# Kernel tuning notes

Measured on AMD Instinct MI355X. Metric: run time of the kernel, lower is better.

Reference implementation:

```python
import jax, jax.numpy as jnp
import numpy as np

N_NODES = 100000
N_EDGES = 1600000
IN_DIM = 256
HID = 128
ALPHA = 0.1
K_STEPS = 10


def setup_inputs() -> dict:
    key = jax.random.key(0)
    ks = jax.random.split(key, 10)
    x = jax.random.normal(ks[0], (N_NODES, IN_DIM), dtype=jnp.float32)
    edge_index = jax.random.randint(ks[1], (2, N_EDGES), 0, N_NODES, dtype=jnp.int64)
    s = 0.02
    W1 = jax.random.normal(ks[2], (HID, IN_DIM), dtype=jnp.float32) * s
    b1 = jnp.zeros((HID,), dtype=jnp.float32)
    W2 = jax.random.normal(ks[3], (HID, HID), dtype=jnp.float32) * s
    b2 = jnp.zeros((HID,), dtype=jnp.float32)
    W3 = jax.random.normal(ks[4], (HID, HID), dtype=jnp.float32) * s
    b3 = jnp.zeros((HID,), dtype=jnp.float32)
    Wo = jax.random.normal(ks[5], (1, HID), dtype=jnp.float32) * s
    bo = jnp.zeros((1,), dtype=jnp.float32)
    return {"x": x, "edge_index": edge_index, "W1": W1, "b1": b1,
            "W2": W2, "b2": b2, "W3": W3, "b3": b3, "Wo": Wo, "bo": bo}


def _gcn_norm(edge_index, num_nodes):
    # add self-loops, then symmetric normalization 1/sqrt(deg_i * deg_j)
    loop = jnp.arange(num_nodes, dtype=edge_index.dtype)
    src = jnp.concatenate([edge_index[0], loop])
    dst = jnp.concatenate([edge_index[1], loop])
    ones = jnp.ones(src.shape[0], dtype=jnp.float32)
    deg = jax.ops.segment_sum(ones, dst, num_segments=num_nodes)
    dinv = jnp.where(deg > 0, jax.lax.rsqrt(deg), 0.0)
    norm = dinv[src] * dinv[dst]
    return src, dst, norm


def reference(x, edge_index, W1, b1, W2, b2, W3, b3, Wo, bo):
    # MLP encoder (dropout=0 -> identity in eval)
    h = jax.nn.relu(x @ W1.T + b1)
    h = jax.nn.relu(h @ W2.T + b2)
    h = jax.nn.relu(h @ W3.T + b3)
    # APPNP propagation: h <- (1-alpha) * A_hat h + alpha * h0
    n = x.shape[0]
    src, dst, norm = _gcn_norm(edge_index, n)
    h0 = h
    for _ in range(K_STEPS):
        msg = norm[:, None] * h[src]            # [E+N, HID]
        agg = jax.ops.segment_sum(msg, dst, num_segments=n)
        h = (1.0 - ALPHA) * agg + ALPHA * h0
    out = h @ Wo.T + bo                          # [N, 1]
    return out.squeeze(-1)
```

## Files before the change

kernel.cpp:

```cpp
#include <hip/hip_runtime.h>

#define NN   100000
#define NE   1600000
#define IND  256
#define HIDD 128
#define BCAP 64
#define NPART 196
#define SCAP 10240
#define APITCH 40
#define HPITCH 136

typedef __attribute__((ext_vector_type(8))) short short8v;
typedef __attribute__((ext_vector_type(4))) float f32x4;

__device__ inline unsigned packbf2(float x, float y) {
  unsigned xb = __float_as_uint(x);
  unsigned yb = __float_as_uint(y);
  xb += 0x7fffu + ((xb >> 16) & 1u);
  yb += 0x7fffu + ((yb >> 16) & 1u);
  return (xb >> 16) | (yb & 0xffff0000u);
}
__device__ inline unsigned short bf16r(float x) {
  unsigned b = __float_as_uint(x);
  b += 0x7fffu + ((b >> 16) & 1u);
  return (unsigned short)(b >> 16);
}

__global__ void wcvt_all(const float* __restrict__ W1, const float* __restrict__ W2,
                         const float* __restrict__ W3, unsigned* __restrict__ W1b,
                         unsigned* __restrict__ W2b, unsigned* __restrict__ W3b) {
  int i = blockIdx.x * 256 + threadIdx.x;
  const float* src; unsigned* dst; int off;
  if (i < 16384)      { src = W1; dst = W1b; off = i; }
  else if (i < 24576) { src = W2; dst = W2b; off = i - 16384; }
  else                { src = W3; dst = W3b; off = i - 24576; }
  float2 v = ((const float2*)src)[off];
  dst[off] = packbf2(v.x, v.y);
}

__global__ __launch_bounds__(256, 8) void fill_phaseA(
    const int* __restrict__ src, const int* __restrict__ dst,
    int* __restrict__ gcur, unsigned* __restrict__ sbuf)
{
  __shared__ int hist[NPART];
  __shared__ int lofs[NPART];
  const int tid = threadIdx.x;
  const int base = blockIdx.x * 2048;
  for (int i = tid; i < NPART; i += 256) hist[i] = 0;
  __syncthreads();
  int d[8], s[8];
#pragma unroll
  for (int i = 0; i < 8; ++i) {
    int e = base + i * 256 + tid;
    bool v = e < NE;
    d[i] = v ? dst[e] : -1;
    s[i] = v ? src[e] : 0;
    if (v) atomicAdd(&hist[d[i] >> 9], 1);
  }
  __syncthreads();
  for (int i = tid; i < NPART; i += 256)
    lofs[i] = hist[i] ? atomicAdd(&gcur[i], hist[i]) : 0;
  __syncthreads();
#pragma unroll
  for (int i = 0; i < 8; ++i) {
    if (d[i] >= 0) {
      int p = d[i] >> 9;
      int q = atomicAdd(&lofs[p], 1);
      if (q < SCAP)
        sbuf[(size_t)p * SCAP + q] = ((unsigned)(d[i] & 511) << 17) | (unsigned)s[i];
    }
  }
}

__global__ __launch_bounds__(256, 8) void fill_phaseB(
    const unsigned* __restrict__ sbuf, const int* __restrict__ gcur,
    int* __restrict__ colbuk, int* __restrict__ deg, float* __restrict__ dinv)
{
  __shared__ int lcur[512];
  const int tid = threadIdx.x;
  const int b = blockIdx.x;
  for (int i = tid; i < 512; i += 256) lcur[i] = 0;
  __syncthreads();
  int cnt = min(gcur[b], SCAP);
  const unsigned* sp = sbuf + (size_t)b * SCAP;
  for (int i = tid; i < cnt; i += 256) {
    unsigned u = sp[i];
    int dloc = (int)(u >> 17);
    int s = (int)(u & 0x1FFFFu);
    int pos = atomicAdd(&lcur[dloc], 1);
    if (pos < BCAP) colbuk[(size_t)((b << 9) + dloc) * BCAP + pos] = s;
  }
  __syncthreads();
  for (int i = tid; i < 512; i += 256) {
    int node = (b << 9) + i;
    if (node < NN) {
      int dg = lcur[i];
      deg[node] = dg;
      dinv[node] = rsqrtf((float)(dg + 1));
    }
  }
}

__global__ __launch_bounds__(256) void enc_fused(
    const float* __restrict__ x,
    const unsigned short* __restrict__ W1b, const float* __restrict__ b1,
    const unsigned short* __restrict__ W2b, const float* __restrict__ b2,
    const unsigned short* __restrict__ W3b, const float* __restrict__ b3,
    const float* __restrict__ Wo, const float* __restrict__ dinv,
    float* __restrict__ z, float* __restrict__ va)
{
  __shared__ unsigned short hbuf[64 * HPITCH];
  __shared__ float zsh[2][64];
  unsigned short* lA = hbuf;
  const int tid = threadIdx.x;
  const int lane = tid & 63, wid = tid >> 6;
  const int wr = wid >> 1, wc = wid & 1;
  const int bm = blockIdx.x * 64;
  const int lr = lane & 15, lg = lane >> 4;

  f32x4 acc[2][4];
#pragma unroll
  for (int i = 0; i < 2; ++i)
#pragma unroll
    for (int j = 0; j < 4; ++j) acc[i][j] = (f32x4){0.f, 0.f, 0.f, 0.f};

  for (int k0 = 0; k0 < IND; k0 += 32) {
    {
      int rr = tid >> 2, g = tid & 3;
      int grow = bm + rr;
      float4 v0 = make_float4(0.f, 0.f, 0.f, 0.f), v1 = v0;
      if (grow < NN) {
        const float* ap = x + (size_t)grow * IND + k0 + g * 8;
        v0 = ((const float4*)ap)[0]; v1 = ((const float4*)ap)[1];
      }
      uint4 pk;
      pk.x = packbf2(v0.x, v0.y); pk.y = packbf2(v0.z, v0.w);
      pk.z = packbf2(v1.x, v1.y); pk.w = packbf2(v1.z, v1.w);
      *(uint4*)&lA[rr * APITCH + g * 8] = pk;
    }
    __syncthreads();
    {
      short8v a[2], b[4];
#pragma unroll
      for (int i = 0; i < 2; ++i)
        a[i] = *(const short8v*)&lA[(wr * 32 + i * 16 + lr) * APITCH + lg * 8];
#pragma unroll
      for (int j = 0; j < 4; ++j)
        b[j] = *(const short8v*)&W1b[(size_t)(wc * 64 + j * 16 + lr) * IND + k0 + lg * 8];
#pragma unroll
      for (int i = 0; i < 2; ++i)
#pragma unroll
        for (int j = 0; j < 4; ++j)
          acc[i][j] = __builtin_amdgcn_mfma_f32_16x16x32_bf16(a[i], b[j], acc[i][j], 0, 0, 0);
    }
    __syncthreads();
  }
#pragma unroll
  for (int i = 0; i < 2; ++i)
#pragma unroll
    for (int e = 0; e < 4; ++e) {
      int lrow = wr * 32 + i * 16 + lg * 4 + e;
#pragma unroll
      for (int j = 0; j < 4; ++j) {
        int cc = wc * 64 + j * 16 + lr;
        hbuf[lrow * HPITCH + cc] = bf16r(fmaxf(acc[i][j][e] + b1[cc], 0.f));
      }
    }
  __syncthreads();

#pragma unroll
  for (int i = 0; i < 2; ++i)
#pragma unroll
    for (int j = 0; j < 4; ++j) acc[i][j] = (f32x4){0.f, 0.f, 0.f, 0.f};
  for (int k0 = 0; k0 < HIDD; k0 += 32) {
    short8v a[2], b[4];
#pragma unroll
    for (int i = 0; i < 2; ++i)
      a[i] = *(const short8v*)&hbuf[(wr * 32 + i * 16 + lr) * HPITCH + k0 + lg * 8];
#pragma unroll
    for (int j = 0; j < 4; ++j)
      b[j] = *(const short8v*)&W2b[(size_t)(wc * 64 + j * 16 + lr) * HIDD + k0 + lg * 8];
#pragma unroll
    for (int i = 0; i < 2; ++i)
#pragma unroll
      for (int j = 0; j < 4; ++j)
        acc[i][j] = __builtin_amdgcn_mfma_f32_16x16x32_bf16(a[i], b[j], acc[i][j], 0, 0, 0);
  }
  __syncthreads();
#pragma unroll
  for (int i = 0; i < 2; ++i)
#pragma unroll
    for (int e = 0; e < 4; ++e) {
      int lrow = wr * 32 + i * 16 + lg * 4 + e;
#pragma unroll
      for (int j = 0; j < 4; ++j) {
        int cc = wc * 64 + j * 16 + lr;
        hbuf[lrow * HPITCH + cc] = bf16r(fmaxf(acc[i][j][e] + b2[cc], 0.f));
      }
    }
  __syncthreads();

#pragma unroll
  for (int i = 0; i < 2; ++i)
#pragma unroll
    for (int j = 0; j < 4; ++j) acc[i][j] = (f32x4){0.f, 0.f, 0.f, 0.f};
  for (int k0 = 0; k0 < HIDD; k0 += 32) {
    short8v a[2], b[4];
#pragma unroll
    for (int i = 0; i < 2; ++i)
      a[i] = *(const short8v*)&hbuf[(wr * 32 + i * 16 + lr) * HPITCH + k0 + lg * 8];
#pragma unroll
    for (int j = 0; j < 4; ++j)
      b[j] = *(const short8v*)&W3b[(size_t)(wc * 64 + j * 16 + lr) * HIDD + k0 + lg * 8];
#pragma unroll
    for (int i = 0; i < 2; ++i)
#pragma unroll
      for (int j = 0; j < 4; ++j)
        acc[i][j] = __builtin_amdgcn_mfma_f32_16x16x32_bf16(a[i], b[j], acc[i][j], 0, 0, 0);
  }
  float wv[4];
#pragma unroll
  for (int j = 0; j < 4; ++j) wv[j] = Wo[wc * 64 + j * 16 + lr];
  if (tid < 128) { zsh[tid >> 6][tid & 63] = 0.f; }
  __syncthreads();
#pragma unroll
  for (int i = 0; i < 2; ++i)
#pragma unroll
    for (int e = 0; e < 4; ++e) {
      float part = 0.f;
#pragma unroll
      for (int j = 0; j < 4; ++j) {
        int cc = wc * 64 + j * 16 + lr;
        part += fmaxf(acc[i][j][e] + b3[cc], 0.f) * wv[j];
      }
#pragma unroll
      for (int off = 8; off > 0; off >>= 1) part += __shfl_down(part, off, 16);
      if (lr == 0) zsh[wc][wr * 32 + i * 16 + lg * 4 + e] = part;
    }
  __syncthreads();
  if (tid < 64) {
    int row = bm + tid;
    if (row < NN) {
      float zv = zsh[0][tid] + zsh[1][tid];
      z[row] = zv;
      va[row] = dinv[row] * zv;
    }
  }
}

template<int LAST>
__global__ __launch_bounds__(256, 8) void appnp_sstep(
    const float* __restrict__ vin, const float* __restrict__ z,
    const float* __restrict__ dinv, const int* __restrict__ deg,
    const int* __restrict__ colbuk, float* __restrict__ vout,
    const float* __restrict__ bo, float* __restrict__ out)
{
  int tid = threadIdx.x;
  int sl = tid & 15;
  int node = blockIdx.x * 16 + (tid >> 4);
  if (node >= NN) return;
  int m = min(deg[node], BCAP);
  float val = (sl == 0) ? vin[node] : 0.f;
  for (int j = sl; j < m; j += 16)
    val += vin[colbuk[(size_t)node * BCAP + j]];
#pragma unroll
  for (int off = 8; off > 0; off >>= 1) val += __shfl_down(val, off, 16);
  if (sl == 0) {
    float di = dinv[node];
    float s = 0.9f * di * val + 0.1f * z[node];
    if (LAST) out[node] = s + bo[0];
    else vout[node] = di * s;
  }
}

extern "C" void kernel_launch(void* const* d_in, const int* in_sizes, int n_in,
                              void* d_out, int out_size, void* d_ws, size_t ws_size,
                              hipStream_t stream) {
  const float* x   = (const float*)d_in[0];
  const int*   ei  = (const int*)d_in[1];
  const float* W1  = (const float*)d_in[2];
  const float* b1  = (const float*)d_in[3];
  const float* W2  = (const float*)d_in[4];
  const float* b2  = (const float*)d_in[5];
  const float* W3  = (const float*)d_in[6];
  const float* b3  = (const float*)d_in[7];
  const float* Wo  = (const float*)d_in[8];
  const float* bo  = (const float*)d_in[9];
  float* out = (float*)d_out;

  const int* srcv = ei;
  const int* dstv = ei + NE;

  int*      colbuk = (int*)d_ws;
  unsigned* sbuf   = (unsigned*)(colbuk + (size_t)NN * BCAP);
  int*      gcur   = (int*)(sbuf + (size_t)NPART * SCAP);
  int*      deg    = gcur + NPART;
  float*    dinv   = (float*)(deg + NN);
  float*    zbuf   = dinv + NN;
  float*    va     = zbuf + NN;
  float*    vb     = va + NN;
  unsigned* W1b    = (unsigned*)(vb + NN);
  unsigned* W2b    = W1b + 16384;
  unsigned* W3b    = W2b + 8192;

  hipMemsetAsync(gcur, 0, NPART * 4, stream);

  wcvt_all<<<128, 256, 0, stream>>>(W1, W2, W3, W1b, W2b, W3b);

  fill_phaseA<<<(NE + 2047) / 2048, 256, 0, stream>>>(srcv, dstv, gcur, sbuf);
  fill_phaseB<<<NPART, 256, 0, stream>>>(sbuf, gcur, colbuk, deg, dinv);

  const int ng = (NN + 63) / 64;
  enc_fused<<<ng, 256, 0, stream>>>(x, (unsigned short*)W1b, b1,
                                    (unsigned short*)W2b, b2,
                                    (unsigned short*)W3b, b3, Wo, dinv,
                                    zbuf, va);

  int ssb = (NN + 15) / 16;
  float* cur = va; float* nxt = vb;
  for (int k = 0; k < 9; ++k) {
    appnp_sstep<0><<<ssb, 256, 0, stream>>>(cur, zbuf, dinv, deg, colbuk,
                                            nxt, nullptr, nullptr);
    float* t = cur; cur = nxt; nxt = t;
  }
  appnp_sstep<1><<<ssb, 256, 0, stream>>>(cur, zbuf, dinv, deg, colbuk,
                                          nullptr, bo, out);
}
```

Measured before the change: 223.8 us.

## Fuse encoder MLP with edge-bucketing phase A into one interleaved launch

Merges the encoder MLP kernel and the first edge-partitioning kernel into one launch. Every third block does edge histogram/scatter work and the other two run MLP tiles, so memory-bound scatter overlaps with MFMA-bound encoder work. The encoder no longer depends on dinv. The dinv*z scaling moves into fill_phaseB, which now runs after the encoder. The fused kernel carries both kernels' shared memory and register needs, which may lower occupancy for the scatter blocks.

```diff
diff --git a/kernel.cpp b/kernel.cpp
--- a/kernel.cpp
+++ b/kernel.cpp
@@ -9,6 +9,8 @@
 #define SCAP 10240
 #define APITCH 40
 #define HPITCH 136
+#define NGE  1563
+#define NFA  782
 
 typedef __attribute__((ext_vector_type(8))) short short8v;
 typedef __attribute__((ext_vector_type(4))) float f32x4;
@@ -38,43 +40,191 @@
   dst[off] = packbf2(v.x, v.y);
 }
 
-__global__ __launch_bounds__(256, 8) void fill_phaseA(
+__global__ __launch_bounds__(256) void enc_fillA(
+    const float* __restrict__ x,
+    const unsigned short* __restrict__ W1b, const float* __restrict__ b1,
+    const unsigned short* __restrict__ W2b, const float* __restrict__ b2,
+    const unsigned short* __restrict__ W3b, const float* __restrict__ b3,
+    const float* __restrict__ Wo, float* __restrict__ z,
     const int* __restrict__ src, const int* __restrict__ dst,
     int* __restrict__ gcur, unsigned* __restrict__ sbuf)
 {
+  __shared__ unsigned short hbuf[64 * HPITCH];
+  __shared__ float zsh[2][64];
   __shared__ int hist[NPART];
   __shared__ int lofs[NPART];
   const int tid = threadIdx.x;
-  const int base = blockIdx.x * 2048;
-  for (int i = tid; i < NPART; i += 256) hist[i] = 0;
-  __syncthreads();
-  int d[8], s[8];
-#pragma unroll
-  for (int i = 0; i < 8; ++i) {
-    int e = base + i * 256 + tid;
-    bool v = e < NE;
-    d[i] = v ? dst[e] : -1;
-    s[i] = v ? src[e] : 0;
-    if (v) atomicAdd(&hist[d[i] >> 9], 1);
-  }
-  __syncthreads();
-  for (int i = tid; i < NPART; i += 256)
-    lofs[i] = hist[i] ? atomicAdd(&gcur[i], hist[i]) : 0;
-  __syncthreads();
-#pragma unroll
-  for (int i = 0; i < 8; ++i) {
-    if (d[i] >= 0) {
-      int p = d[i] >> 9;
-      int q = atomicAdd(&lofs[p], 1);
-      if (q < SCAP)
-        sbuf[(size_t)p * SCAP + q] = ((unsigned)(d[i] & 511) << 17) | (unsigned)s[i];
-    }
+  const int bid = blockIdx.x;
+  const int r3v = bid % 3;
+
+  if (r3v == 2) {
+    int fi = bid / 3;
+    const int base = fi * 2048;
+    for (int i = tid; i < NPART; i += 256) hist[i] = 0;
+    __syncthreads();
+    int d[8], s[8];
+#pragma unroll
+    for (int i = 0; i < 8; ++i) {
+      int e = base + i * 256 + tid;
+      bool v = e < NE;
+      d[i] = v ? dst[e] : -1;
+      s[i] = v ? src[e] : 0;
+      if (v) atomicAdd(&hist[d[i] >> 9], 1);
+    }
+    __syncthreads();
+    for (int i = tid; i < NPART; i += 256)
+      lofs[i] = hist[i] ? atomicAdd(&gcur[i], hist[i]) : 0;
+    __syncthreads();
+#pragma unroll
+    for (int i = 0; i < 8; ++i) {
+      if (d[i] >= 0) {
+        int p = d[i] >> 9;
+        int q = atomicAdd(&lofs[p], 1);
+        if (q < SCAP)
+          sbuf[(size_t)p * SCAP + q] = ((unsigned)(d[i] & 511) << 17) | (unsigned)s[i];
+      }
+    }
+    return;
+  }
+
+  const int gb = (bid / 3) * 2 + r3v;
+  if (gb >= NGE) return;
+  unsigned short* lA = hbuf;
+  const int lane = tid & 63, wid = tid >> 6;
+  const int wr = wid >> 1, wc = wid & 1;
+  const int bm = gb * 64;
+  const int lr = lane & 15, lg = lane >> 4;
+
+  f32x4 acc[2][4];
+#pragma unroll
+  for (int i = 0; i < 2; ++i)
+#pragma unroll
+    for (int j = 0; j < 4; ++j) acc[i][j] = (f32x4){0.f, 0.f, 0.f, 0.f};
+
+  for (int k0 = 0; k0 < IND; k0 += 32) {
+    {
+      int rr = tid >> 2, g = tid & 3;
+      int grow = bm + rr;
+      float4 v0 = make_float4(0.f, 0.f, 0.f, 0.f), v1 = v0;
+      if (grow < NN) {
+        const float* ap = x + (size_t)grow * IND + k0 + g * 8;
+        v0 = ((const float4*)ap)[0]; v1 = ((const float4*)ap)[1];
+      }
+      uint4 pk;
+      pk.x = packbf2(v0.x, v0.y); pk.y = packbf2(v0.z, v0.w);
+      pk.z = packbf2(v1.x, v1.y); pk.w = packbf2(v1.z, v1.w);
+      *(uint4*)&lA[rr * APITCH + g * 8] = pk;
+    }
+    __syncthreads();
+    {
+      short8v a[2], b[4];
+#pragma unroll
+      for (int i = 0; i < 2; ++i)
+        a[i] = *(const short8v*)&lA[(wr * 32 + i * 16 + lr) * APITCH + lg * 8];
+#pragma unroll
+      for (int j = 0; j < 4; ++j)
+        b[j] = *(const short8v*)&W1b[(size_t)(wc * 64 + j * 16 + lr) * IND + k0 + lg * 8];
+#pragma unroll
+      for (int i = 0; i < 2; ++i)
+#pragma unroll
+        for (int j = 0; j < 4; ++j)
+          acc[i][j] = __builtin_amdgcn_mfma_f32_16x16x32_bf16(a[i], b[j], acc[i][j], 0, 0, 0);
+    }
+    __syncthreads();
+  }
+#pragma unroll
+  for (int i = 0; i < 2; ++i)
+#pragma unroll
+    for (int e = 0; e < 4; ++e) {
+      int lrow = wr * 32 + i * 16 + lg * 4 + e;
+#pragma unroll
+      for (int j = 0; j < 4; ++j) {
+        int cc = wc * 64 + j * 16 + lr;
+        hbuf[lrow * HPITCH + cc] = bf16r(fmaxf(acc[i][j][e] + b1[cc], 0.f));
+      }
+    }
+  __syncthreads();
+
+#pragma unroll
+  for (int i = 0; i < 2; ++i)
+#pragma unroll
+    for (int j = 0; j < 4; ++j) acc[i][j] = (f32x4){0.f, 0.f, 0.f, 0.f};
+  for (int k0 = 0; k0 < HIDD; k0 += 32) {
+    short8v a[2], b[4];
+#pragma unroll
+    for (int i = 0; i < 2; ++i)
+      a[i] = *(const short8v*)&hbuf[(wr * 32 + i * 16 + lr) * HPITCH + k0 + lg * 8];
+#pragma unroll
+    for (int j = 0; j < 4; ++j)
+      b[j] = *(const short8v*)&W2b[(size_t)(wc * 64 + j * 16 + lr) * HIDD + k0 + lg * 8];
+#pragma unroll
+    for (int i = 0; i < 2; ++i)
+#pragma unroll
+      for (int j = 0; j < 4; ++j)
+        acc[i][j] = __builtin_amdgcn_mfma_f32_16x16x32_bf16(a[i], b[j], acc[i][j], 0, 0, 0);
+  }
+  __syncthreads();
+#pragma unroll
+  for (int i = 0; i < 2; ++i)
+#pragma unroll
+    for (int e = 0; e < 4; ++e) {
+      int lrow = wr * 32 + i * 16 + lg * 4 + e;
+#pragma unroll
+      for (int j = 0; j < 4; ++j) {
+        int cc = wc * 64 + j * 16 + lr;
+        hbuf[lrow * HPITCH + cc] = bf16r(fmaxf(acc[i][j][e] + b2[cc], 0.f));
+      }
+    }
+  __syncthreads();
+
+#pragma unroll
+  for (int i = 0; i < 2; ++i)
+#pragma unroll
+    for (int j = 0; j < 4; ++j) acc[i][j] = (f32x4){0.f, 0.f, 0.f, 0.f};
+  for (int k0 = 0; k0 < HIDD; k0 += 32) {
+    short8v a[2], b[4];
+#pragma unroll
+    for (int i = 0; i < 2; ++i)
+      a[i] = *(const short8v*)&hbuf[(wr * 32 + i * 16 + lr) * HPITCH + k0 + lg * 8];
+#pragma unroll
+    for (int j = 0; j < 4; ++j)
+      b[j] = *(const short8v*)&W3b[(size_t)(wc * 64 + j * 16 + lr) * HIDD + k0 + lg * 8];
+#pragma unroll
+    for (int i = 0; i < 2; ++i)
+#pragma unroll
+      for (int j = 0; j < 4; ++j)
+        acc[i][j] = __builtin_amdgcn_mfma_f32_16x16x32_bf16(a[i], b[j], acc[i][j], 0, 0, 0);
+  }
+  float wv[4];
+#pragma unroll
+  for (int j = 0; j < 4; ++j) wv[j] = Wo[wc * 64 + j * 16 + lr];
+  if (tid < 128) { zsh[tid >> 6][tid & 63] = 0.f; }
+  __syncthreads();
+#pragma unroll
+  for (int i = 0; i < 2; ++i)
+#pragma unroll
+    for (int e = 0; e < 4; ++e) {
+      float part = 0.f;
+#pragma unroll
+      for (int j = 0; j < 4; ++j) {
+        int cc = wc * 64 + j * 16 + lr;
+        part += fmaxf(acc[i][j][e] + b3[cc], 0.f) * wv[j];
+      }
+#pragma unroll
+      for (int off = 8; off > 0; off >>= 1) part += __shfl_down(part, off, 16);
+      if (lr == 0) zsh[wc][wr * 32 + i * 16 + lg * 4 + e] = part;
+    }
+  __syncthreads();
+  if (tid < 64) {
+    int row = bm + tid;
+    if (row < NN) z[row] = zsh[0][tid] + zsh[1][tid];
   }
 }
 
 __global__ __launch_bounds__(256, 8) void fill_phaseB(
     const unsigned* __restrict__ sbuf, const int* __restrict__ gcur,
-    int* __restrict__ colbuk, int* __restrict__ deg, float* __restrict__ dinv)
+    const float* __restrict__ z, int* __restrict__ colbuk,
+    int* __restrict__ deg, float* __restrict__ dinv, float* __restrict__ va)
 {
   __shared__ int lcur[512];
   const int tid = threadIdx.x;
@@ -95,155 +245,10 @@
     int node = (b << 9) + i;
     if (node < NN) {
       int dg = lcur[i];
+      float di = rsqrtf((float)(dg + 1));
       deg[node] = dg;
-      dinv[node] = rsqrtf((float)(dg + 1));
-    }
-  }
-}
-
-__global__ __launch_bounds__(256) void enc_fused(
-    const float* __restrict__ x,
-    const unsigned short* __restrict__ W1b, const float* __restrict__ b1,
-    const unsigned short* __restrict__ W2b, const float* __restrict__ b2,
-    const unsigned short* __restrict__ W3b, const float* __restrict__ b3,
-    const float* __restrict__ Wo, const float* __restrict__ dinv,
-    float* __restrict__ z, float* __restrict__ va)
-{
-  __shared__ unsigned short hbuf[64 * HPITCH];
-  __shared__ float zsh[2][64];
-  unsigned short* lA = hbuf;
-  const int tid = threadIdx.x;
-  const int lane = tid & 63, wid = tid >> 6;
-  const int wr = wid >> 1, wc = wid & 1;
-  const int bm = blockIdx.x * 64;
-  const int lr = lane & 15, lg = lane >> 4;
-
-  f32x4 acc[2][4];
-#pragma unroll
-  for (int i = 0; i < 2; ++i)
-#pragma unroll
-    for (int j = 0; j < 4; ++j) acc[i][j] = (f32x4){0.f, 0.f, 0.f, 0.f};
-
-  for (int k0 = 0; k0 < IND; k0 += 32) {
-    {
-      int rr = tid >> 2, g = tid & 3;
-      int grow = bm + rr;
-      float4 v0 = make_float4(0.f, 0.f, 0.f, 0.f), v1 = v0;
-      if (grow < NN) {
-        const float* ap = x + (size_t)grow * IND + k0 + g * 8;
-        v0 = ((const float4*)ap)[0]; v1 = ((const float4*)ap)[1];
-      }
-      uint4 pk;
-      pk.x = packbf2(v0.x, v0.y); pk.y = packbf2(v0.z, v0.w);
-      pk.z = packbf2(v1.x, v1.y); pk.w = packbf2(v1.z, v1.w);
-      *(uint4*)&lA[rr * APITCH + g * 8] = pk;
-    }
-    __syncthreads();
-    {
-      short8v a[2], b[4];
-#pragma unroll
-      for (int i = 0; i < 2; ++i)
-        a[i] = *(const short8v*)&lA[(wr * 32 + i * 16 + lr) * APITCH + lg * 8];
-#pragma unroll
-      for (int j = 0; j < 4; ++j)
-        b[j] = *(const short8v*)&W1b[(size_t)(wc * 64 + j * 16 + lr) * IND + k0 + lg * 8];
-#pragma unroll
-      for (int i = 0; i < 2; ++i)
-#pragma unroll
-        for (int j = 0; j < 4; ++j)
-          acc[i][j] = __builtin_amdgcn_mfma_f32_16x16x32_bf16(a[i], b[j], acc[i][j], 0, 0, 0);
-    }
-    __syncthreads();
-  }
-#pragma unroll
-  for (int i = 0; i < 2; ++i)
-#pragma unroll
-    for (int e = 0; e < 4; ++e) {
-      int lrow = wr * 32 + i * 16 + lg * 4 + e;
-#pragma unroll
-      for (int j = 0; j < 4; ++j) {
-        int cc = wc * 64 + j * 16 + lr;
-        hbuf[lrow * HPITCH + cc] = bf16r(fmaxf(acc[i][j][e] + b1[cc], 0.f));
-      }
-    }
-  __syncthreads();
-
-#pragma unroll
-  for (int i = 0; i < 2; ++i)
-#pragma unroll
-    for (int j = 0; j < 4; ++j) acc[i][j] = (f32x4){0.f, 0.f, 0.f, 0.f};
-  for (int k0 = 0; k0 < HIDD; k0 += 32) {
-    short8v a[2], b[4];
-#pragma unroll
-    for (int i = 0; i < 2; ++i)
-      a[i] = *(const short8v*)&hbuf[(wr * 32 + i * 16 + lr) * HPITCH + k0 + lg * 8];
-#pragma unroll
-    for (int j = 0; j < 4; ++j)
-      b[j] = *(const short8v*)&W2b[(size_t)(wc * 64 + j * 16 + lr) * HIDD + k0 + lg * 8];
-#pragma unroll
-    for (int i = 0; i < 2; ++i)
-#pragma unroll
-      for (int j = 0; j < 4; ++j)
-        acc[i][j] = __builtin_amdgcn_mfma_f32_16x16x32_bf16(a[i], b[j], acc[i][j], 0, 0, 0);
-  }
-  __syncthreads();
-#pragma unroll
-  for (int i = 0; i < 2; ++i)
-#pragma unroll
-    for (int e = 0; e < 4; ++e) {
-      int lrow = wr * 32 + i * 16 + lg * 4 + e;
-#pragma unroll
-      for (int j = 0; j < 4; ++j) {
-        int cc = wc * 64 + j * 16 + lr;
-        hbuf[lrow * HPITCH + cc] = bf16r(fmaxf(acc[i][j][e] + b2[cc], 0.f));
-      }
-    }
-  __syncthreads();
-
-#pragma unroll
-  for (int i = 0; i < 2; ++i)
-#pragma unroll
-    for (int j = 0; j < 4; ++j) acc[i][j] = (f32x4){0.f, 0.f, 0.f, 0.f};
-  for (int k0 = 0; k0 < HIDD; k0 += 32) {
-    short8v a[2], b[4];
-#pragma unroll
-    for (int i = 0; i < 2; ++i)
-      a[i] = *(const short8v*)&hbuf[(wr * 32 + i * 16 + lr) * HPITCH + k0 + lg * 8];
-#pragma unroll
-    for (int j = 0; j < 4; ++j)
-      b[j] = *(const short8v*)&W3b[(size_t)(wc * 64 + j * 16 + lr) * HIDD + k0 + lg * 8];
-#pragma unroll
-    for (int i = 0; i < 2; ++i)
-#pragma unroll
-      for (int j = 0; j < 4; ++j)
-        acc[i][j] = __builtin_amdgcn_mfma_f32_16x16x32_bf16(a[i], b[j], acc[i][j], 0, 0, 0);
-  }
-  float wv[4];
-#pragma unroll
-  for (int j = 0; j < 4; ++j) wv[j] = Wo[wc * 64 + j * 16 + lr];
-  if (tid < 128) { zsh[tid >> 6][tid & 63] = 0.f; }
-  __syncthreads();
-#pragma unroll
-  for (int i = 0; i < 2; ++i)
-#pragma unroll
-    for (int e = 0; e < 4; ++e) {
-      float part = 0.f;
-#pragma unroll
-      for (int j = 0; j < 4; ++j) {
-        int cc = wc * 64 + j * 16 + lr;
-        part += fmaxf(acc[i][j][e] + b3[cc], 0.f) * wv[j];
-      }
-#pragma unroll
-      for (int off = 8; off > 0; off >>= 1) part += __shfl_down(part, off, 16);
-      if (lr == 0) zsh[wc][wr * 32 + i * 16 + lg * 4 + e] = part;
-    }
-  __syncthreads();
-  if (tid < 64) {
-    int row = bm + tid;
-    if (row < NN) {
-      float zv = zsh[0][tid] + zsh[1][tid];
-      z[row] = zv;
-      va[row] = dinv[row] * zv;
+      dinv[node] = di;
+      va[node] = di * z[node];
     }
   }
 }
@@ -307,14 +312,12 @@
 
   wcvt_all<<<128, 256, 0, stream>>>(W1, W2, W3, W1b, W2b, W3b);
 
-  fill_phaseA<<<(NE + 2047) / 2048, 256, 0, stream>>>(srcv, dstv, gcur, sbuf);
-  fill_phaseB<<<NPART, 256, 0, stream>>>(sbuf, gcur, colbuk, deg, dinv);
-
-  const int ng = (NN + 63) / 64;
-  enc_fused<<<ng, 256, 0, stream>>>(x, (unsigned short*)W1b, b1,
-                                    (unsigned short*)W2b, b2,
-                                    (unsigned short*)W3b, b3, Wo, dinv,
-                                    zbuf, va);
+  enc_fillA<<<2346, 256, 0, stream>>>(x, (unsigned short*)W1b, b1,
+                                      (unsigned short*)W2b, b2,
+                                      (unsigned short*)W3b, b3, Wo, zbuf,
+                                      srcv, dstv, gcur, sbuf);
+
+  fill_phaseB<<<NPART, 256, 0, stream>>>(sbuf, gcur, zbuf, colbuk, deg, dinv, va);
 
   int ssb = (NN + 15) / 16;
   float* cur = va; float* nxt = vb;
```

Result: faster. 207.6 us (-7.2%).
